# Kernel optimization log

Hardware: AMD Instinct MI355X
Metric: run time of the kernel (lower is better)

The kernel has to match this reference:

```python
import jax, jax.numpy as jnp
import numpy as np

C = 256
NUM_HEADS = 4
REDUCTION = 4
RED = C // REDUCTION           # 64
HEAD_DIM = RED // NUM_HEADS    # 16
SCALE = HEAD_DIM ** -0.5
LN_EPS = 1e-5


def setup_inputs() -> dict:
    key = jax.random.key(0)
    ks = jax.random.split(key, 9)
    B, H, W = 2, 64, 64
    x = jax.random.normal(ks[0], (B, C, H, W), dtype=jnp.float32)
    # LayerNorm params
    norm_w = jnp.ones((C,), jnp.float32)
    norm_b = jnp.zeros((C,), jnp.float32)
    # Linear weights (torch layout: [out, in]), y = x @ W.T
    qkv_w = jax.random.normal(ks[1], (3 * RED, C), jnp.float32) * (C ** -0.5)
    out_w = jax.random.normal(ks[2], (C, RED), jnp.float32) * (RED ** -0.5)
    # 1x1 conv weights, stored as [out_c, in_c]
    conv1_w = jax.random.normal(ks[3], (C // 2, C), jnp.float32) * (C ** -0.5)
    conv1_b = jax.random.normal(ks[4], (C // 2,), jnp.float32) * 0.01
    conv2_w = jax.random.normal(ks[5], (1, C // 2), jnp.float32) * ((C // 2) ** -0.5)
    conv2_b = jax.random.normal(ks[6], (1,), jnp.float32) * 0.01
    gamma = jnp.ones((1,), jnp.float32) * 0.5  # nonzero so output depends on attention
    return {"x": x, "norm_w": norm_w, "norm_b": norm_b, "qkv_w": qkv_w,
            "out_w": out_w, "conv1_w": conv1_w, "conv1_b": conv1_b,
            "conv2_w": conv2_w, "conv2_b": conv2_b, "gamma": gamma}


def reference(x, norm_w, norm_b, qkv_w, out_w, conv1_w, conv1_b, conv2_w, conv2_b, gamma):
    B, C_, H, W = x.shape
    N = H * W
    # [B, N, C]
    xf = x.reshape(B, C_, N).transpose(0, 2, 1)
    # LayerNorm over channel dim
    mu = jnp.mean(xf, axis=-1, keepdims=True)
    var = jnp.mean(jnp.square(xf - mu), axis=-1, keepdims=True)
    xn = (xf - mu) * jax.lax.rsqrt(var + LN_EPS) * norm_w + norm_b
    # QKV projection -> [B, N, 3*RED]
    qkv = jnp.einsum('bnc,oc->bno', xn, qkv_w)
    q, k, v = jnp.split(qkv, 3, axis=-1)
    def heads(t):  # [B, N, RED] -> [B, h, N, d]
        return t.reshape(B, N, NUM_HEADS, HEAD_DIM).transpose(0, 2, 1, 3)
    q, k, v = heads(q), heads(k), heads(v)
    attn = jax.nn.softmax(jnp.einsum('bhnd,bhmd->bhnm', q, k) * SCALE, axis=-1)
    # dynamic weight branch: two 1x1 convs on raw x
    d1 = jax.nn.relu(jnp.einsum('oc,bchw->bohw', conv1_w, x) + conv1_b[None, :, None, None])
    dyn = (jnp.einsum('oc,bchw->bohw', conv2_w, d1) + conv2_b[None, :, None, None])  # [B,1,H,W]
    dyn = dyn.reshape(B, 1, N)  # broadcast over heads
    # per-query row scaling of attention
    attn = attn * dyn[:, :, :, None]
    out = jnp.einsum('bhnm,bhmd->bhnd', attn, v)            # [B,h,N,d]
    out = out.transpose(0, 2, 1, 3).reshape(B, N, RED)      # [B,N,RED]
    out = jnp.einsum('bnr,cr->bnc', out, out_w)             # [B,N,C]
    out = out.transpose(0, 2, 1).reshape(B, C_, H, W)
    return jax.nn.sigmoid(gamma[0] * out + x)
```

## Files before the change

kernel.cpp:

```cpp
#include <hip/hip_runtime.h>
#include <cstdint>
#include <cstddef>

#define LOG2E 1.44269504088896340736f

typedef float  f32x16 __attribute__((ext_vector_type(16)));
typedef __bf16 bf16x8 __attribute__((ext_vector_type(8)));

union BF8 { bf16x8 v; uint u[4]; ushort us[8]; };

__device__ __forceinline__ uint pack_bf(float a, float b) {
    uint ua = __float_as_uint(a) + 0x8000u;
    uint ub = __float_as_uint(b) + 0x8000u;
    return __builtin_amdgcn_perm(ub, ua, 0x07060302u);
}
__device__ __forceinline__ float bf_lo(uint u) { return __uint_as_float(u << 16); }
__device__ __forceinline__ float bf_hi(uint u) { return __uint_as_float(u & 0xFFFF0000u); }

__global__ __launch_bounds__(256) void convert_w_kernel(
    const float* __restrict__ qkv_w, const float* __restrict__ c1w,
    const float* __restrict__ out_w,
    ushort* __restrict__ qkvw_b, ushort* __restrict__ c1w_b, ushort* __restrict__ ow_b)
{
    const int g = (blockIdx.x * 256 + threadIdx.x) * 4;
    const float* src; ushort* dst; int off; float sc = 1.f;
    if (g < 49152)      { src = qkv_w; dst = qkvw_b; off = g;
                          if (g < 16384) sc = 0.25f * LOG2E; }
    else if (g < 81920) { src = c1w;   dst = c1w_b;  off = g - 49152; }
    else                { src = out_w; dst = ow_b;   off = g - 81920; }
    float4 v = *(const float4*)(src + off);
    uint2 pk;
    pk.x = pack_bf(v.x * sc, v.y * sc);
    pk.y = pack_bf(v.z * sc, v.w * sc);
    *(uint2*)(dst + off) = pk;
}

__global__ __launch_bounds__(256) void lnqkv_kernel(
    const float* __restrict__ x, const float* __restrict__ nw, const float* __restrict__ nb,
    const ushort* __restrict__ qkvw_b, const ushort* __restrict__ c1w_b,
    const float* __restrict__ c1b, const float* __restrict__ c2w,
    const float* __restrict__ c2b,
    ushort* __restrict__ Qb, ushort* __restrict__ Kb, ushort* __restrict__ Vsw,
    float* __restrict__ dynb)
{
    __shared__ uint  XN[32 * 32 * 4];
    __shared__ uint  XR[32 * 32 * 4];
    __shared__ float trans[4][32 * 33];
    __shared__ float red1[256], red2[256];
    __shared__ float muS[32], rsS[32];

    const int t    = threadIdx.x;
    const int pg   = blockIdx.x;
    const int b    = pg >> 7;
    const int n0   = (pg & 127) * 32;

    {
        const int j  = t & 31;
        const int cg = t >> 5;
        const size_t xb = (size_t)b * 256 * 4096 + n0 + j;
        float v[32];
        #pragma unroll
        for (int i = 0; i < 32; ++i) v[i] = x[xb + (size_t)(cg * 32 + i) * 4096];
        float s1 = 0.f, s2 = 0.f;
        #pragma unroll
        for (int i = 0; i < 32; ++i) { s1 += v[i]; s2 += v[i] * v[i]; }
        #pragma unroll
        for (int kk = 0; kk < 4; ++kk) {
            uint4 pk;
            pk.x = pack_bf(v[kk * 8 + 0], v[kk * 8 + 1]);
            pk.y = pack_bf(v[kk * 8 + 2], v[kk * 8 + 3]);
            pk.z = pack_bf(v[kk * 8 + 4], v[kk * 8 + 5]);
            pk.w = pack_bf(v[kk * 8 + 6], v[kk * 8 + 7]);
            *(uint4*)&XR[((cg * 4 + kk) * 32 + j) * 4] = pk;
        }
        red1[t] = s1; red2[t] = s2;
        __syncthreads();
        if (t < 32) {
            float a = 0.f, q = 0.f;
            #pragma unroll
            for (int g2 = 0; g2 < 8; ++g2) { a += red1[g2 * 32 + t]; q += red2[g2 * 32 + t]; }
            float mu  = a * (1.f / 256.f);
            float var = q * (1.f / 256.f) - mu * mu;
            muS[t] = mu; rsS[t] = rsqrtf(fmaxf(var, 0.f) + 1e-5f);
        }
        __syncthreads();
        const float mu = muS[j], rs = rsS[j];
        #pragma unroll
        for (int kk = 0; kk < 4; ++kk) {
            const float4 w0 = *(const float4*)(nw + cg * 32 + kk * 8);
            const float4 w1 = *(const float4*)(nw + cg * 32 + kk * 8 + 4);
            const float4 b0 = *(const float4*)(nb + cg * 32 + kk * 8);
            const float4 b1 = *(const float4*)(nb + cg * 32 + kk * 8 + 4);
            float e0 = (v[kk * 8 + 0] - mu) * rs * w0.x + b0.x;
            float e1 = (v[kk * 8 + 1] - mu) * rs * w0.y + b0.y;
            float e2 = (v[kk * 8 + 2] - mu) * rs * w0.z + b0.z;
            float e3 = (v[kk * 8 + 3] - mu) * rs * w0.w + b0.w;
            float e4 = (v[kk * 8 + 4] - mu) * rs * w1.x + b1.x;
            float e5 = (v[kk * 8 + 5] - mu) * rs * w1.y + b1.y;
            float e6 = (v[kk * 8 + 6] - mu) * rs * w1.z + b1.z;
            float e7 = (v[kk * 8 + 7] - mu) * rs * w1.w + b1.w;
            uint4 o;
            o.x = pack_bf(e0, e1); o.y = pack_bf(e2, e3);
            o.z = pack_bf(e4, e5); o.w = pack_bf(e6, e7);
            *(uint4*)&XN[((cg * 4 + kk) * 32 + j) * 4] = o;
        }
    }
    __syncthreads();

    const int w    = t >> 6;
    const int lane = t & 63;
    const int m    = lane & 31;
    const int h    = lane >> 5;
    float* tr = trans[w];
    const ushort* xnB = (const ushort*)XN;
    const ushort* xrB = (const ushort*)XR;

    if (w < 3) {
        const ushort* ap0 = qkvw_b + ((size_t)(w * 64 + m)) * 256 + h * 8;
        const ushort* ap1 = ap0 + 32 * 256;
        f32x16 acc0, acc1;
        #pragma unroll
        for (int i = 0; i < 16; ++i) { acc0[i] = 0.f; acc1[i] = 0.f; }
        #pragma unroll 4
        for (int ks = 0; ks < 16; ++ks) {
            bf16x8 bf = *(const bf16x8*)(xnB + ((ks * 2 + h) * 32 + m) * 8);
            bf16x8 a0 = *(const bf16x8*)(ap0 + ks * 16);
            bf16x8 a1 = *(const bf16x8*)(ap1 + ks * 16);
            acc0 = __builtin_amdgcn_mfma_f32_32x32x16_bf16(a0, bf, acc0, 0, 0, 0);
            acc1 = __builtin_amdgcn_mfma_f32_32x32x16_bf16(a1, bf, acc1, 0, 0, 0);
        }
        for (int ti = 0; ti < 2; ++ti) {
            const f32x16& A = ti ? acc1 : acc0;
            #pragma unroll
            for (int r = 0; r < 16; ++r)
                tr[((r & 3) + 8 * (r >> 2) + 4 * h) * 33 + m] = A[r];
            if (w < 2) {
                ushort* dst = (w == 0) ? Qb : Kb;
                #pragma unroll
                for (int it = 0; it < 2; ++it) {
                    int unit = it * 2 + h;
                    int hl = unit >> 1, half = unit & 1;
                    float v0 = tr[(hl * 16 + half * 8 + 0) * 33 + m];
                    float v1 = tr[(hl * 16 + half * 8 + 1) * 33 + m];
                    float v2 = tr[(hl * 16 + half * 8 + 2) * 33 + m];
                    float v3 = tr[(hl * 16 + half * 8 + 3) * 33 + m];
                    float v4 = tr[(hl * 16 + half * 8 + 4) * 33 + m];
                    float v5 = tr[(hl * 16 + half * 8 + 5) * 33 + m];
                    float v6 = tr[(hl * 16 + half * 8 + 6) * 33 + m];
                    float v7 = tr[(hl * 16 + half * 8 + 7) * 33 + m];
                    uint4 pk;
                    pk.x = pack_bf(v0, v1); pk.y = pack_bf(v2, v3);
                    pk.z = pack_bf(v4, v5); pk.w = pack_bf(v6, v7);
                    int head = ti * 2 + hl;
                    *(uint4*)(dst + ((size_t)(b * 4 + head) * 4096 + n0 + m) * 16 + half * 8) = pk;
                }
            } else {
                int d = lane & 15, u = lane >> 4;
                #pragma unroll
                for (int it = 0; it < 4; ++it) {
                    int unit = it * 4 + u;
                    int hl = unit >> 3, sg = unit & 7;
                    float v0 = tr[(hl * 16 + d) * 33 + sg * 4 + 0];
                    float v1 = tr[(hl * 16 + d) * 33 + sg * 4 + 1];
                    float v2 = tr[(hl * 16 + d) * 33 + sg * 4 + 2];
                    float v3 = tr[(hl * 16 + d) * 33 + sg * 4 + 3];
                    uint2 pk; pk.x = pack_bf(v0, v1); pk.y = pack_bf(v2, v3);
                    int head = ti * 2 + hl;
                    *(uint2*)(Vsw + (((size_t)(b * 4 + head) * 1024 + (pg & 127) * 8 + sg) * 16 + d) * 4) = pk;
                }
            }
        }
    } else {
        f32x16 acc[4];
        #pragma unroll
        for (int ti = 0; ti < 4; ++ti)
            #pragma unroll
            for (int i = 0; i < 16; ++i) acc[ti][i] = 0.f;
        #pragma unroll 2
        for (int ks = 0; ks < 16; ++ks) {
            bf16x8 bf = *(const bf16x8*)(xrB + ((ks * 2 + h) * 32 + m) * 8);
            #pragma unroll
            for (int ti = 0; ti < 4; ++ti) {
                bf16x8 a = *(const bf16x8*)(c1w_b + ((size_t)(ti * 32 + m)) * 256 + ks * 16 + h * 8);
                acc[ti] = __builtin_amdgcn_mfma_f32_32x32x16_bf16(a, bf, acc[ti], 0, 0, 0);
            }
        }
        float partial = 0.f;
        for (int ti = 0; ti < 4; ++ti) {
            #pragma unroll
            for (int r = 0; r < 16; ++r)
                tr[((r & 3) + 8 * (r >> 2) + 4 * h) * 33 + m] = acc[ti][r];
            #pragma unroll
            for (int i = 0; i < 16; ++i) {
                int og = ti * 32 + h * 16 + i;
                partial += fmaxf(tr[(h * 16 + i) * 33 + m] + c1b[og], 0.f) * c2w[og];
            }
        }
        float tot = partial + __shfl_xor(partial, 32);
        if (lane < 32) dynb[(size_t)b * 4096 + n0 + m] = c2b[0] + tot;
    }
}

__global__ __launch_bounds__(1024) void attn_final_kernel(
    const ushort* __restrict__ Qb, const ushort* __restrict__ Kb,
    const ushort* __restrict__ Vsw, const float* __restrict__ dynb,
    const ushort* __restrict__ ow_b, const float* __restrict__ x,
    const float* __restrict__ gamma, float* __restrict__ out)
{
    __shared__ float2 OM[4][4][8][32];
    __shared__ float  LM[4][4][32];

    const int t    = threadIdx.x;
    const int w    = t >> 6;
    const int lane = t & 63;
    const int c    = lane & 31;
    const int h    = lane >> 5;
    const int hd   = w & 3;
    const int kb   = w >> 2;
    const int pg   = blockIdx.x;
    const int b    = pg >> 7;
    const int n0   = (pg & 127) * 32;
    const int bh   = b * 4 + hd;

    const bf16x8 qf = *(const bf16x8*)(Qb + ((size_t)bh * 4096 + n0 + c) * 16 + h * 8);

    f32x16 oacc, zf;
    #pragma unroll
    for (int i = 0; i < 16; ++i) { oacc[i] = 0.f; zf[i] = 0.f; }

    const ushort* kp = Kb + ((size_t)bh * 4096 + kb * 1024 + c) * 16 + h * 8;
    const ushort* vb = Vsw + (size_t)bh * 65536 + ((size_t)kb * 256 + h) * 64 + c * 4;

    #pragma unroll 2
    for (int ch = 0; ch < 32; ++ch) {
        const bf16x8 kf = *(const bf16x8*)kp;
        f32x16 s = __builtin_amdgcn_mfma_f32_32x32x16_bf16(kf, qf, zf, 0, 0, 0);

        BF8 p1, p2;
        #pragma unroll
        for (int jj = 0; jj < 4; ++jj) {
            p1.u[jj] = pack_bf(__builtin_amdgcn_exp2f(s[2*jj]),   __builtin_amdgcn_exp2f(s[2*jj+1]));
            p2.u[jj] = pack_bf(__builtin_amdgcn_exp2f(s[8+2*jj]), __builtin_amdgcn_exp2f(s[8+2*jj+1]));
        }

        BF8 a1, a2;
        if (c < 16) {
            const uint2 g1 = *(const uint2*)(vb);
            const uint2 g2 = *(const uint2*)(vb + 128);
            const uint2 g3 = *(const uint2*)(vb + 256);
            const uint2 g4 = *(const uint2*)(vb + 384);
            a1.u[0] = g1.x; a1.u[1] = g1.y; a1.u[2] = g2.x; a1.u[3] = g2.y;
            a2.u[0] = g3.x; a2.u[1] = g3.y; a2.u[2] = g4.x; a2.u[3] = g4.y;
        } else {
            const uint f = (c == 16) ? 0x3F803F80u : 0u;
            a1.u[0] = a1.u[1] = a1.u[2] = a1.u[3] = f;
            a2.u[0] = a2.u[1] = a2.u[2] = a2.u[3] = f;
        }

        oacc = __builtin_amdgcn_mfma_f32_32x32x16_bf16(a1.v, p1.v, oacc, 0, 0, 0);
        oacc = __builtin_amdgcn_mfma_f32_32x32x16_bf16(a2.v, p2.v, oacc, 0, 0, 0);

        kp += 512; vb += 512;
    }

    OM[kb][hd][2 * h + 0][c] = make_float2(oacc[0], oacc[1]);
    OM[kb][hd][2 * h + 1][c] = make_float2(oacc[2], oacc[3]);
    OM[kb][hd][4 + 2 * h][c] = make_float2(oacc[4], oacc[5]);
    OM[kb][hd][5 + 2 * h][c] = make_float2(oacc[6], oacc[7]);
    if (h == 0) LM[kb][hd][c] = oacc[8];
    __syncthreads();

    if (w < 8) {
        const int m = c;
        const float dyn_px = dynb[(size_t)b * 4096 + n0 + m];

        f32x16 acc;
        #pragma unroll
        for (int i = 0; i < 16; ++i) acc[i] = 0.f;

        #pragma unroll
        for (int ks = 0; ks < 4; ++ks) {
            float l = LM[0][ks][m] + LM[1][ks][m] + LM[2][ks][m] + LM[3][ks][m];
            float fac = dyn_px / l;
            BF8 bfr;
            #pragma unroll
            for (int i = 0; i < 4; ++i) {
                int sl = 4 * h + i;
                float2 s0 = OM[0][ks][sl][m];
                float2 s1 = OM[1][ks][sl][m];
                float2 s2 = OM[2][ks][sl][m];
                float2 s3 = OM[3][ks][sl][m];
                float e0 = (s0.x + s1.x + s2.x + s3.x) * fac;
                float e1 = (s0.y + s1.y + s2.y + s3.y) * fac;
                bfr.u[i] = pack_bf(e0, e1);
            }
            bf16x8 af = *(const bf16x8*)(ow_b + (size_t)(w * 32 + m) * 64 + ks * 16 + h * 8);
            acc = __builtin_amdgcn_mfma_f32_32x32x16_bf16(af, bfr.v, acc, 0, 0, 0);
        }

        const float g = gamma[0];
        #pragma unroll
        for (int r = 0; r < 16; ++r) {
            int o = (r & 3) + 8 * (r >> 2) + 4 * h;
            size_t idx = ((size_t)b * 256 + w * 32 + o) * 4096 + n0 + m;
            float z = g * acc[r] + x[idx];
            out[idx] = 1.f / (1.f + __builtin_amdgcn_exp2f(-z * LOG2E));
        }
    }
}

extern "C" void kernel_launch(void* const* d_in, const int* in_sizes, int n_in,
                              void* d_out, int out_size, void* d_ws, size_t ws_size,
                              hipStream_t stream)
{
    const float* x      = (const float*)d_in[0];
    const float* norm_w = (const float*)d_in[1];
    const float* norm_b = (const float*)d_in[2];
    const float* qkv_w  = (const float*)d_in[3];
    const float* out_w  = (const float*)d_in[4];
    const float* c1w    = (const float*)d_in[5];
    const float* c1b    = (const float*)d_in[6];
    const float* c2w    = (const float*)d_in[7];
    const float* c2b    = (const float*)d_in[8];
    const float* gamma  = (const float*)d_in[9];

    char* ws = (char*)d_ws;
    ushort* Qb     = (ushort*)ws;
    ushort* Kb     = Qb + 524288;
    ushort* Vsw    = Kb + 524288;
    ushort* qkvw_b = Vsw + 524288;
    ushort* c1w_b  = qkvw_b + 49152;
    ushort* ow_b   = c1w_b + 32768;
    float*  dynb   = (float*)(ws + 3342336);

    hipLaunchKernelGGL(convert_w_kernel, dim3(96), dim3(256), 0, stream,
                       qkv_w, c1w, out_w, qkvw_b, c1w_b, ow_b);
    hipLaunchKernelGGL(lnqkv_kernel, dim3(256), dim3(256), 0, stream,
                       x, norm_w, norm_b, qkvw_b, c1w_b, c1b, c2w, c2b,
                       Qb, Kb, Vsw, dynb);
    hipLaunchKernelGGL(attn_final_kernel, dim3(256), dim3(1024), 0, stream,
                       Qb, Kb, Vsw, dynb, ow_b, x, gamma, (float*)d_out);
}
```

Measured before the change: 114.5 us.

## Fuse weight bf16 conversion into consumers and widen LN/QKV kernel to 1024 threads

Removes the separate weight-conversion kernel launch: the QKV, conv1 and output-projection weights are now read as fp32 and packed to bf16 inline before each MFMA. The LN/QKV kernel grows from 256 to 1024 threads per block, with each wave computing one 32-row output tile and the dyn partial sums reduced through shared memory. Shared buffers are unioned to fit the larger block. The trade is one fewer launch and more waves for latency hiding, against doubled weight read bytes and repeated conversion work in every block.

```diff
diff --git a/kernel.cpp b/kernel.cpp
--- a/kernel.cpp
+++ b/kernel.cpp
@@ -17,37 +17,25 @@
 __device__ __forceinline__ float bf_lo(uint u) { return __uint_as_float(u << 16); }
 __device__ __forceinline__ float bf_hi(uint u) { return __uint_as_float(u & 0xFFFF0000u); }
 
-__global__ __launch_bounds__(256) void convert_w_kernel(
+__global__ __launch_bounds__(1024) void lnqkv_kernel(
+    const float* __restrict__ x, const float* __restrict__ nw, const float* __restrict__ nb,
     const float* __restrict__ qkv_w, const float* __restrict__ c1w,
-    const float* __restrict__ out_w,
-    ushort* __restrict__ qkvw_b, ushort* __restrict__ c1w_b, ushort* __restrict__ ow_b)
-{
-    const int g = (blockIdx.x * 256 + threadIdx.x) * 4;
-    const float* src; ushort* dst; int off; float sc = 1.f;
-    if (g < 49152)      { src = qkv_w; dst = qkvw_b; off = g;
-                          if (g < 16384) sc = 0.25f * LOG2E; }
-    else if (g < 81920) { src = c1w;   dst = c1w_b;  off = g - 49152; }
-    else                { src = out_w; dst = ow_b;   off = g - 81920; }
-    float4 v = *(const float4*)(src + off);
-    uint2 pk;
-    pk.x = pack_bf(v.x * sc, v.y * sc);
-    pk.y = pack_bf(v.z * sc, v.w * sc);
-    *(uint2*)(dst + off) = pk;
-}
-
-__global__ __launch_bounds__(256) void lnqkv_kernel(
-    const float* __restrict__ x, const float* __restrict__ nw, const float* __restrict__ nb,
-    const ushort* __restrict__ qkvw_b, const ushort* __restrict__ c1w_b,
     const float* __restrict__ c1b, const float* __restrict__ c2w,
     const float* __restrict__ c2b,
     ushort* __restrict__ Qb, ushort* __restrict__ Kb, ushort* __restrict__ Vsw,
     float* __restrict__ dynb)
 {
-    __shared__ uint  XN[32 * 32 * 4];
-    __shared__ uint  XR[32 * 32 * 4];
-    __shared__ float trans[4][32 * 33];
-    __shared__ float red1[256], red2[256];
+    __shared__ union {
+        struct {
+            uint  XN[32 * 32 * 4];
+            uint  XR[32 * 32 * 4];
+            float red1[1024];
+            float red2[1024];
+        } p;
+        float trans[10][33 * 32];
+    } S;
     __shared__ float muS[32], rsS[32];
+    __shared__ float dpart[4][32];
 
     const int t    = threadIdx.x;
     const int pg   = blockIdx.x;
@@ -58,52 +46,44 @@
         const int j  = t & 31;
         const int cg = t >> 5;
         const size_t xb = (size_t)b * 256 * 4096 + n0 + j;
-        float v[32];
-        #pragma unroll
-        for (int i = 0; i < 32; ++i) v[i] = x[xb + (size_t)(cg * 32 + i) * 4096];
+        float v[8];
+        #pragma unroll
+        for (int i = 0; i < 8; ++i) v[i] = x[xb + (size_t)(cg * 8 + i) * 4096];
         float s1 = 0.f, s2 = 0.f;
         #pragma unroll
-        for (int i = 0; i < 32; ++i) { s1 += v[i]; s2 += v[i] * v[i]; }
-        #pragma unroll
-        for (int kk = 0; kk < 4; ++kk) {
-            uint4 pk;
-            pk.x = pack_bf(v[kk * 8 + 0], v[kk * 8 + 1]);
-            pk.y = pack_bf(v[kk * 8 + 2], v[kk * 8 + 3]);
-            pk.z = pack_bf(v[kk * 8 + 4], v[kk * 8 + 5]);
-            pk.w = pack_bf(v[kk * 8 + 6], v[kk * 8 + 7]);
-            *(uint4*)&XR[((cg * 4 + kk) * 32 + j) * 4] = pk;
-        }
-        red1[t] = s1; red2[t] = s2;
+        for (int i = 0; i < 8; ++i) { s1 += v[i]; s2 += v[i] * v[i]; }
+        uint4 pk;
+        pk.x = pack_bf(v[0], v[1]); pk.y = pack_bf(v[2], v[3]);
+        pk.z = pack_bf(v[4], v[5]); pk.w = pack_bf(v[6], v[7]);
+        *(uint4*)&S.p.XR[(cg * 32 + j) * 4] = pk;
+        S.p.red1[t] = s1; S.p.red2[t] = s2;
         __syncthreads();
         if (t < 32) {
             float a = 0.f, q = 0.f;
-            #pragma unroll
-            for (int g2 = 0; g2 < 8; ++g2) { a += red1[g2 * 32 + t]; q += red2[g2 * 32 + t]; }
+            #pragma unroll 8
+            for (int g2 = 0; g2 < 32; ++g2) { a += S.p.red1[g2 * 32 + t]; q += S.p.red2[g2 * 32 + t]; }
             float mu  = a * (1.f / 256.f);
             float var = q * (1.f / 256.f) - mu * mu;
             muS[t] = mu; rsS[t] = rsqrtf(fmaxf(var, 0.f) + 1e-5f);
         }
         __syncthreads();
         const float mu = muS[j], rs = rsS[j];
-        #pragma unroll
-        for (int kk = 0; kk < 4; ++kk) {
-            const float4 w0 = *(const float4*)(nw + cg * 32 + kk * 8);
-            const float4 w1 = *(const float4*)(nw + cg * 32 + kk * 8 + 4);
-            const float4 b0 = *(const float4*)(nb + cg * 32 + kk * 8);
-            const float4 b1 = *(const float4*)(nb + cg * 32 + kk * 8 + 4);
-            float e0 = (v[kk * 8 + 0] - mu) * rs * w0.x + b0.x;
-            float e1 = (v[kk * 8 + 1] - mu) * rs * w0.y + b0.y;
-            float e2 = (v[kk * 8 + 2] - mu) * rs * w0.z + b0.z;
-            float e3 = (v[kk * 8 + 3] - mu) * rs * w0.w + b0.w;
-            float e4 = (v[kk * 8 + 4] - mu) * rs * w1.x + b1.x;
-            float e5 = (v[kk * 8 + 5] - mu) * rs * w1.y + b1.y;
-            float e6 = (v[kk * 8 + 6] - mu) * rs * w1.z + b1.z;
-            float e7 = (v[kk * 8 + 7] - mu) * rs * w1.w + b1.w;
-            uint4 o;
-            o.x = pack_bf(e0, e1); o.y = pack_bf(e2, e3);
-            o.z = pack_bf(e4, e5); o.w = pack_bf(e6, e7);
-            *(uint4*)&XN[((cg * 4 + kk) * 32 + j) * 4] = o;
-        }
+        const float4 w0 = *(const float4*)(nw + cg * 8);
+        const float4 w1 = *(const float4*)(nw + cg * 8 + 4);
+        const float4 b0 = *(const float4*)(nb + cg * 8);
+        const float4 b1 = *(const float4*)(nb + cg * 8 + 4);
+        float e0 = (v[0] - mu) * rs * w0.x + b0.x;
+        float e1 = (v[1] - mu) * rs * w0.y + b0.y;
+        float e2 = (v[2] - mu) * rs * w0.z + b0.z;
+        float e3 = (v[3] - mu) * rs * w0.w + b0.w;
+        float e4 = (v[4] - mu) * rs * w1.x + b1.x;
+        float e5 = (v[5] - mu) * rs * w1.y + b1.y;
+        float e6 = (v[6] - mu) * rs * w1.z + b1.z;
+        float e7 = (v[7] - mu) * rs * w1.w + b1.w;
+        uint4 o;
+        o.x = pack_bf(e0, e1); o.y = pack_bf(e2, e3);
+        o.z = pack_bf(e4, e5); o.w = pack_bf(e6, e7);
+        *(uint4*)&S.p.XN[(cg * 32 + j) * 4] = o;
     }
     __syncthreads();
 
@@ -111,100 +91,112 @@
     const int lane = t & 63;
     const int m    = lane & 31;
     const int h    = lane >> 5;
-    float* tr = trans[w];
-    const ushort* xnB = (const ushort*)XN;
-    const ushort* xrB = (const ushort*)XR;
-
-    if (w < 3) {
-        const ushort* ap0 = qkvw_b + ((size_t)(w * 64 + m)) * 256 + h * 8;
-        const ushort* ap1 = ap0 + 32 * 256;
-        f32x16 acc0, acc1;
-        #pragma unroll
-        for (int i = 0; i < 16; ++i) { acc0[i] = 0.f; acc1[i] = 0.f; }
+    const ushort* xnB = (const ushort*)S.p.XN;
+    const ushort* xrB = (const ushort*)S.p.XR;
+
+    f32x16 acc;
+    #pragma unroll
+    for (int i = 0; i < 16; ++i) acc[i] = 0.f;
+
+    if (w < 6) {
+        const int qkv = w >> 1;
+        const int ti  = w & 1;
+        const float sc = (qkv == 0) ? 0.25f * LOG2E : 1.f;
+        const float* ap = qkv_w + (size_t)(qkv * 64 + ti * 32 + m) * 256 + h * 8;
         #pragma unroll 4
         for (int ks = 0; ks < 16; ++ks) {
             bf16x8 bf = *(const bf16x8*)(xnB + ((ks * 2 + h) * 32 + m) * 8);
-            bf16x8 a0 = *(const bf16x8*)(ap0 + ks * 16);
-            bf16x8 a1 = *(const bf16x8*)(ap1 + ks * 16);
-            acc0 = __builtin_amdgcn_mfma_f32_32x32x16_bf16(a0, bf, acc0, 0, 0, 0);
-            acc1 = __builtin_amdgcn_mfma_f32_32x32x16_bf16(a1, bf, acc1, 0, 0, 0);
-        }
-        for (int ti = 0; ti < 2; ++ti) {
-            const f32x16& A = ti ? acc1 : acc0;
-            #pragma unroll
-            for (int r = 0; r < 16; ++r)
-                tr[((r & 3) + 8 * (r >> 2) + 4 * h) * 33 + m] = A[r];
-            if (w < 2) {
-                ushort* dst = (w == 0) ? Qb : Kb;
-                #pragma unroll
-                for (int it = 0; it < 2; ++it) {
-                    int unit = it * 2 + h;
-                    int hl = unit >> 1, half = unit & 1;
-                    float v0 = tr[(hl * 16 + half * 8 + 0) * 33 + m];
-                    float v1 = tr[(hl * 16 + half * 8 + 1) * 33 + m];
-                    float v2 = tr[(hl * 16 + half * 8 + 2) * 33 + m];
-                    float v3 = tr[(hl * 16 + half * 8 + 3) * 33 + m];
-                    float v4 = tr[(hl * 16 + half * 8 + 4) * 33 + m];
-                    float v5 = tr[(hl * 16 + half * 8 + 5) * 33 + m];
-                    float v6 = tr[(hl * 16 + half * 8 + 6) * 33 + m];
-                    float v7 = tr[(hl * 16 + half * 8 + 7) * 33 + m];
-                    uint4 pk;
-                    pk.x = pack_bf(v0, v1); pk.y = pack_bf(v2, v3);
-                    pk.z = pack_bf(v4, v5); pk.w = pack_bf(v6, v7);
-                    int head = ti * 2 + hl;
-                    *(uint4*)(dst + ((size_t)(b * 4 + head) * 4096 + n0 + m) * 16 + half * 8) = pk;
-                }
-            } else {
-                int d = lane & 15, u = lane >> 4;
-                #pragma unroll
-                for (int it = 0; it < 4; ++it) {
-                    int unit = it * 4 + u;
-                    int hl = unit >> 3, sg = unit & 7;
-                    float v0 = tr[(hl * 16 + d) * 33 + sg * 4 + 0];
-                    float v1 = tr[(hl * 16 + d) * 33 + sg * 4 + 1];
-                    float v2 = tr[(hl * 16 + d) * 33 + sg * 4 + 2];
-                    float v3 = tr[(hl * 16 + d) * 33 + sg * 4 + 3];
-                    uint2 pk; pk.x = pack_bf(v0, v1); pk.y = pack_bf(v2, v3);
-                    int head = ti * 2 + hl;
-                    *(uint2*)(Vsw + (((size_t)(b * 4 + head) * 1024 + (pg & 127) * 8 + sg) * 16 + d) * 4) = pk;
-                }
-            }
-        }
-    } else {
-        f32x16 acc[4];
-        #pragma unroll
-        for (int ti = 0; ti < 4; ++ti)
-            #pragma unroll
-            for (int i = 0; i < 16; ++i) acc[ti][i] = 0.f;
-        #pragma unroll 2
+            float4 a0 = *(const float4*)(ap + ks * 16);
+            float4 a1 = *(const float4*)(ap + ks * 16 + 4);
+            BF8 af;
+            af.u[0] = pack_bf(a0.x * sc, a0.y * sc);
+            af.u[1] = pack_bf(a0.z * sc, a0.w * sc);
+            af.u[2] = pack_bf(a1.x * sc, a1.y * sc);
+            af.u[3] = pack_bf(a1.z * sc, a1.w * sc);
+            acc = __builtin_amdgcn_mfma_f32_32x32x16_bf16(af.v, bf, acc, 0, 0, 0);
+        }
+    } else if (w < 10) {
+        const int ti = w - 6;
+        const float* ap = c1w + (size_t)(ti * 32 + m) * 256 + h * 8;
+        #pragma unroll 4
         for (int ks = 0; ks < 16; ++ks) {
             bf16x8 bf = *(const bf16x8*)(xrB + ((ks * 2 + h) * 32 + m) * 8);
+            float4 a0 = *(const float4*)(ap + ks * 16);
+            float4 a1 = *(const float4*)(ap + ks * 16 + 4);
+            BF8 af;
+            af.u[0] = pack_bf(a0.x, a0.y);
+            af.u[1] = pack_bf(a0.z, a0.w);
+            af.u[2] = pack_bf(a1.x, a1.y);
+            af.u[3] = pack_bf(a1.z, a1.w);
+            acc = __builtin_amdgcn_mfma_f32_32x32x16_bf16(af.v, bf, acc, 0, 0, 0);
+        }
+    }
+    __syncthreads();
+
+    if (w < 10) {
+        float* tr = S.trans[w];
+        #pragma unroll
+        for (int r = 0; r < 16; ++r)
+            tr[((r & 3) + 8 * (r >> 2) + 4 * h) * 33 + m] = acc[r];
+
+        if (w < 4) {
+            const int qkv = w >> 1, ti = w & 1;
+            ushort* dst = (qkv == 0) ? Qb : Kb;
             #pragma unroll
-            for (int ti = 0; ti < 4; ++ti) {
-                bf16x8 a = *(const bf16x8*)(c1w_b + ((size_t)(ti * 32 + m)) * 256 + ks * 16 + h * 8);
-                acc[ti] = __builtin_amdgcn_mfma_f32_32x32x16_bf16(a, bf, acc[ti], 0, 0, 0);
+            for (int it = 0; it < 2; ++it) {
+                int unit = it * 2 + h;
+                int hl = unit >> 1, half = unit & 1;
+                float v0 = tr[(hl * 16 + half * 8 + 0) * 33 + m];
+                float v1 = tr[(hl * 16 + half * 8 + 1) * 33 + m];
+                float v2 = tr[(hl * 16 + half * 8 + 2) * 33 + m];
+                float v3 = tr[(hl * 16 + half * 8 + 3) * 33 + m];
+                float v4 = tr[(hl * 16 + half * 8 + 4) * 33 + m];
+                float v5 = tr[(hl * 16 + half * 8 + 5) * 33 + m];
+                float v6 = tr[(hl * 16 + half * 8 + 6) * 33 + m];
+                float v7 = tr[(hl * 16 + half * 8 + 7) * 33 + m];
+                uint4 pk;
+                pk.x = pack_bf(v0, v1); pk.y = pack_bf(v2, v3);
+                pk.z = pack_bf(v4, v5); pk.w = pack_bf(v6, v7);
+                int head = ti * 2 + hl;
+                *(uint4*)(dst + ((size_t)(b * 4 + head) * 4096 + n0 + m) * 16 + half * 8) = pk;
             }
-        }
-        float partial = 0.f;
-        for (int ti = 0; ti < 4; ++ti) {
+        } else if (w < 6) {
+            const int ti = w & 1;
+            int d = lane & 15, u = lane >> 4;
             #pragma unroll
-            for (int r = 0; r < 16; ++r)
-                tr[((r & 3) + 8 * (r >> 2) + 4 * h) * 33 + m] = acc[ti][r];
+            for (int it = 0; it < 4; ++it) {
+                int unit = it * 4 + u;
+                int hl = unit >> 3, sg = unit & 7;
+                float v0 = tr[(hl * 16 + d) * 33 + sg * 4 + 0];
+                float v1 = tr[(hl * 16 + d) * 33 + sg * 4 + 1];
+                float v2 = tr[(hl * 16 + d) * 33 + sg * 4 + 2];
+                float v3 = tr[(hl * 16 + d) * 33 + sg * 4 + 3];
+                uint2 pk; pk.x = pack_bf(v0, v1); pk.y = pack_bf(v2, v3);
+                int head = ti * 2 + hl;
+                *(uint2*)(Vsw + (((size_t)(b * 4 + head) * 1024 + (pg & 127) * 8 + sg) * 16 + d) * 4) = pk;
+            }
+        } else {
+            const int ti = w - 6;
+            float partial = 0.f;
             #pragma unroll
             for (int i = 0; i < 16; ++i) {
                 int og = ti * 32 + h * 16 + i;
                 partial += fmaxf(tr[(h * 16 + i) * 33 + m] + c1b[og], 0.f) * c2w[og];
             }
-        }
-        float tot = partial + __shfl_xor(partial, 32);
-        if (lane < 32) dynb[(size_t)b * 4096 + n0 + m] = c2b[0] + tot;
-    }
+            float tot = partial + __shfl_xor(partial, 32);
+            if (lane < 32) dpart[ti][m] = tot;
+        }
+    }
+    __syncthreads();
+    if (t < 32)
+        dynb[(size_t)b * 4096 + n0 + t] =
+            c2b[0] + dpart[0][t] + dpart[1][t] + dpart[2][t] + dpart[3][t];
 }
 
 __global__ __launch_bounds__(1024) void attn_final_kernel(
     const ushort* __restrict__ Qb, const ushort* __restrict__ Kb,
     const ushort* __restrict__ Vsw, const float* __restrict__ dynb,
-    const ushort* __restrict__ ow_b, const float* __restrict__ x,
+    const float* __restrict__ out_w, const float* __restrict__ x,
     const float* __restrict__ gamma, float* __restrict__ out)
 {
     __shared__ float2 OM[4][4][8][32];
@@ -273,6 +265,7 @@
     if (w < 8) {
         const int m = c;
         const float dyn_px = dynb[(size_t)b * 4096 + n0 + m];
+        const float* ap = out_w + (size_t)(w * 32 + m) * 64 + h * 8;
 
         f32x16 acc;
         #pragma unroll
@@ -294,8 +287,14 @@
                 float e1 = (s0.y + s1.y + s2.y + s3.y) * fac;
                 bfr.u[i] = pack_bf(e0, e1);
             }
-            bf16x8 af = *(const bf16x8*)(ow_b + (size_t)(w * 32 + m) * 64 + ks * 16 + h * 8);
-            acc = __builtin_amdgcn_mfma_f32_32x32x16_bf16(af, bfr.v, acc, 0, 0, 0);
+            float4 a0 = *(const float4*)(ap + ks * 16);
+            float4 a1 = *(const float4*)(ap + ks * 16 + 4);
+            BF8 af;
+            af.u[0] = pack_bf(a0.x, a0.y);
+            af.u[1] = pack_bf(a0.z, a0.w);
+            af.u[2] = pack_bf(a1.x, a1.y);
+            af.u[3] = pack_bf(a1.z, a1.w);
+            acc = __builtin_amdgcn_mfma_f32_32x32x16_bf16(af.v, bfr.v, acc, 0, 0, 0);
         }
 
         const float g = gamma[0];
@@ -325,19 +324,14 @@
     const float* gamma  = (const float*)d_in[9];
 
     char* ws = (char*)d_ws;
-    ushort* Qb     = (ushort*)ws;
-    ushort* Kb     = Qb + 524288;
-    ushort* Vsw    = Kb + 524288;
-    ushort* qkvw_b = Vsw + 524288;
-    ushort* c1w_b  = qkvw_b + 49152;
-    ushort* ow_b   = c1w_b + 32768;
-    float*  dynb   = (float*)(ws + 3342336);
-
-    hipLaunchKernelGGL(convert_w_kernel, dim3(96), dim3(256), 0, stream,
-                       qkv_w, c1w, out_w, qkvw_b, c1w_b, ow_b);
-    hipLaunchKernelGGL(lnqkv_kernel, dim3(256), dim3(256), 0, stream,
-                       x, norm_w, norm_b, qkvw_b, c1w_b, c1b, c2w, c2b,
+    ushort* Qb   = (ushort*)ws;
+    ushort* Kb   = Qb + 524288;
+    ushort* Vsw  = Kb + 524288;
+    float*  dynb = (float*)(ws + 3145728);
+
+    hipLaunchKernelGGL(lnqkv_kernel, dim3(256), dim3(1024), 0, stream,
+                       x, norm_w, norm_b, qkv_w, c1w, c1b, c2w, c2b,
                        Qb, Kb, Vsw, dynb);
     hipLaunchKernelGGL(attn_final_kernel, dim3(256), dim3(1024), 0, stream,
-                       Qb, Kb, Vsw, dynb, ow_b, x, gamma, (float*)d_out);
+                       Qb, Kb, Vsw, dynb, out_w, x, gamma, (float*)d_out);
 }
```

Result: slower. 118.3 us (+3.3%).
